# Kernel optimization log

Measured on AMD Instinct MI355X. Metric: run time of the kernel, lower is better.

## Reference

```python
import jax, jax.numpy as jnp
import numpy as np

B, S, D, H = 2, 2048, 1024, 16
HD = D // H  # head_size = 64

def setup_inputs() -> dict:
    key = jax.random.key(0)
    ks = jax.random.split(key, 8)
    sc = 0.02
    return {
        "q": jax.random.normal(ks[0], (B, S, D), jnp.float32),
        "k": jax.random.normal(ks[1], (B, S, D), jnp.float32),
        "v": jax.random.normal(ks[2], (B, S, D), jnp.float32),
        "padding_mask": jnp.zeros((B, 1, 1, S), jnp.float32),
        "Wq": jax.random.normal(ks[3], (D, D), jnp.float32) * sc,
        "bq": jnp.zeros((D,), jnp.float32),
        "Wk": jax.random.normal(ks[4], (D, D), jnp.float32) * sc,
        "bk": jnp.zeros((D,), jnp.float32),
        "Wv": jax.random.normal(ks[5], (D, D), jnp.float32) * sc,
        "bv": jnp.zeros((D,), jnp.float32),
        "Wo": jax.random.normal(ks[6], (D, D), jnp.float32) * sc,
        "bo": jnp.zeros((D,), jnp.float32),
    }

def reference(q, k, v, padding_mask, Wq, bq, Wk, bk, Wv, bv, Wo, bo):
    b = q.shape[0]
    qh = (q @ Wq + bq).reshape(b, -1, H, HD)
    kh = (k @ Wk + bk).reshape(b, -1, H, HD)
    vh = (v @ Wv + bv).reshape(b, -1, H, HD)
    # [B, H, Sq, Sk] scores, materialized as in the original
    qk = jnp.einsum('bjhd,bkhd->bhjk', qh, kh) / jnp.sqrt(jnp.float32(HD))
    qk = qk + padding_mask * -1e12
    attn = jax.nn.softmax(qk, axis=-1)
    qkv = jnp.einsum('bhjk,bkhd->bjhd', attn, vh).reshape(b, -1, D)
    return qkv @ Wo + bo
```

## Files before the change

### kernel.cpp

```cpp
#include <hip/hip_runtime.h>
#include <math.h>

typedef __bf16 bf16_t;
typedef __bf16 bf16x8 __attribute__((ext_vector_type(8)));
typedef __bf16 bf16x4v __attribute__((ext_vector_type(4)));
typedef float f32x4 __attribute__((ext_vector_type(4)));
typedef float f32x16 __attribute__((ext_vector_type(16)));

#define LOG2E 1.4426950408889634f
#define MBIAS_C (-1e12f * LOG2E)

#if __has_builtin(__builtin_amdgcn_exp2f)
#define EXP2F(x) __builtin_amdgcn_exp2f(x)
#else
#define EXP2F(x) exp2f(x)
#endif

typedef __attribute__((address_space(1))) const unsigned int g_u32;
typedef __attribute__((address_space(3))) unsigned int l_u32;
__device__ __forceinline__ void load_lds_16B(const void* g, void* l){
  __builtin_amdgcn_global_load_lds((g_u32*)g, (l_u32*)l, 16, 0, 0);
}

__device__ __forceinline__ f32x16 zero16(){
  f32x16 z;
  #pragma unroll
  for (int i = 0; i < 16; i++) z[i] = 0.f;
  return z;
}

typedef union { bf16x4v b4; uint2 u2; } pk8;
typedef union { uint2 h[2]; bf16x8 b8; } pk16;
typedef union { float4 f4[4]; f32x16 v; } cinit_t;

__global__ __launch_bounds__(256) void cast3_kernel(const float* __restrict__ q,
                                                    const float* __restrict__ k,
                                                    const float* __restrict__ v,
                                                    bf16_t* __restrict__ out){
  int z = blockIdx.y;
  const float* x = (z == 0) ? q : (z == 1) ? k : v;
  int i = blockIdx.x * 256 + threadIdx.x;
  float4 f = reinterpret_cast<const float4*>(x)[i];
  bf16x4v w;
  w[0] = (bf16_t)f.x; w[1] = (bf16_t)f.y; w[2] = (bf16_t)f.z; w[3] = (bf16_t)f.w;
  reinterpret_cast<bf16x4v*>(out + (size_t)z * 4194304)[i] = w;
}

__global__ __launch_bounds__(256) void mask_scale_kernel(const float* __restrict__ mask,
                                                         float* __restrict__ ms){
  int i = blockIdx.x * 256 + threadIdx.x;
  ms[i] = mask[i] * MBIAS_C;
}

__global__ __launch_bounds__(256) void wtrans4_kernel(const float* __restrict__ Wq,
                                                      const float* __restrict__ Wk,
                                                      const float* __restrict__ Wv,
                                                      const float* __restrict__ Wo,
                                                      bf16_t* __restrict__ Wcat,
                                                      bf16_t* __restrict__ Wot){
  __shared__ float T[32][33];
  int z = blockIdx.z;
  const float* W = (z == 0) ? Wq : (z == 1) ? Wk : (z == 2) ? Wv : Wo;
  bf16_t* dst = (z < 3) ? (Wcat + (size_t)z * 1024 * 1024) : Wot;
  int x = threadIdx.x, y = threadIdx.y;
  int k0 = blockIdx.y * 32, n0 = blockIdx.x * 32;
  #pragma unroll
  for (int i = 0; i < 4; i++) T[y + 8*i][x] = W[(size_t)(k0 + y + 8*i) * 1024 + n0 + x];
  __syncthreads();
  #pragma unroll
  for (int i = 0; i < 4; i++) dst[(size_t)(n0 + y + 8*i) * 1024 + k0 + x] = (bf16_t)T[x][y + 8*i];
}

__device__ __forceinline__ void qkv_epilogue(f32x4 (&acc)[4][4], int seg, int n0g, int m0,
                                             int wm, int wn, int l16, int lq,
                                             const float* bias, bf16_t* qp, bf16_t* kp,
                                             bf16_t* vh){
  bf16_t* Cp = (seg == 0) ? qp : (seg == 1) ? kp : vh;
  float scale = (seg == 0) ? 0.125f * LOG2E : 1.0f;
  #pragma unroll
  for (int ti = 0; ti < 4; ti++){
    #pragma unroll
    for (int tj = 0; tj < 4; tj++){
      int col = (n0g + wn + tj*16 + l16) & 1023;
      float bvv = bias[col];
      #pragma unroll
      for (int r = 0; r < 4; r++){
        int row = m0 + wm + ti*16 + lq*4 + r;
        Cp[(size_t)row * 1024 + col] = (bf16_t)((acc[ti][tj][r] + bvv) * scale);
      }
    }
  }
}

__global__ __launch_bounds__(256) void gemm_qkv_bf(const bf16_t* __restrict__ qkvin,
                                                   const bf16_t* __restrict__ Wcat,
                                                   const float* __restrict__ bq,
                                                   const float* __restrict__ bk,
                                                   const float* __restrict__ bv,
                                                   bf16_t* __restrict__ qp,
                                                   bf16_t* __restrict__ kp,
                                                   bf16_t* __restrict__ vh){
  const int K = 1024;
  __shared__ __align__(16) bf16_t As[128*32];
  __shared__ __align__(16) bf16_t Bs[128*32];
  int tid = threadIdx.x, wave = tid >> 6, lane = tid & 63;
  int l16 = lane & 15, lq = lane >> 4;
  int n0g = blockIdx.x * 128;
  int seg = n0g >> 10;
  const bf16_t* A   = qkvin + (size_t)seg * 4194304;
  const float* bias = (seg == 0) ? bq : (seg == 1) ? bk : bv;
  int m0 = blockIdx.y * 128;
  int wm = (wave >> 1) * 64, wn = (wave & 1) * 64;
  int cposR = lq ^ ((l16 >> 2) & 3);
  f32x4 acc[4][4] = {};
  for (int kt = 0; kt < K; kt += 32){
    __syncthreads();
    #pragma unroll
    for (int i = 0; i < 2; i++){
      int u = tid + 256*i;
      int r = u >> 2, cpos = u & 3, cg = cpos ^ ((r >> 2) & 3);
      int ldsoff = (wave*64 + 256*i) * 16;
      load_lds_16B(&A[(size_t)(m0 + r) * K + kt + cg*8], (char*)As + ldsoff);
      load_lds_16B(&Wcat[(size_t)(n0g + r) * K + kt + cg*8], (char*)Bs + ldsoff);
    }
    __syncthreads();
    bf16x8 af[4], bfr[4];
    #pragma unroll
    for (int t = 0; t < 4; t++) af[t]  = *reinterpret_cast<bf16x8*>(&As[(wm + t*16 + l16)*32 + cposR*8]);
    #pragma unroll
    for (int t = 0; t < 4; t++) bfr[t] = *reinterpret_cast<bf16x8*>(&Bs[(wn + t*16 + l16)*32 + cposR*8]);
    #pragma unroll
    for (int ti = 0; ti < 4; ti++)
      #pragma unroll
      for (int tj = 0; tj < 4; tj++)
        acc[ti][tj] = __builtin_amdgcn_mfma_f32_16x16x32_bf16(af[ti], bfr[tj], acc[ti][tj], 0, 0, 0);
  }
  qkv_epilogue(acc, seg, n0g, m0, wm, wn, l16, lq, bias, qp, kp, vh);
}

__global__ __launch_bounds__(256) void gemm_qkv_f32(const float* __restrict__ qi,
                                                    const float* __restrict__ ki,
                                                    const float* __restrict__ vi,
                                                    const bf16_t* __restrict__ Wcat,
                                                    const float* __restrict__ bq,
                                                    const float* __restrict__ bk,
                                                    const float* __restrict__ bv,
                                                    bf16_t* __restrict__ qp,
                                                    bf16_t* __restrict__ kp,
                                                    bf16_t* __restrict__ vh){
  const int K = 1024;
  __shared__ __align__(16) float  Asf[128*32];
  __shared__ __align__(16) bf16_t Bs[128*32];
  int tid = threadIdx.x, wave = tid >> 6, lane = tid & 63;
  int l16 = lane & 15, lq = lane >> 4;
  int n0g = blockIdx.x * 128;
  int seg = n0g >> 10;
  const float* A    = (seg == 0) ? qi : (seg == 1) ? ki : vi;
  const float* bias = (seg == 0) ? bq : (seg == 1) ? bk : bv;
  int m0 = blockIdx.y * 128;
  int wm = (wave >> 1) * 64, wn = (wave & 1) * 64;
  int cposR = lq ^ ((l16 >> 2) & 3);
  int ca0 = (2*lq)     ^ (l16 & 7);
  int ca1 = (2*lq + 1) ^ (l16 & 7);
  f32x4 acc[4][4] = {};
  for (int kt = 0; kt < K; kt += 32){
    __syncthreads();
    #pragma unroll
    for (int i = 0; i < 4; i++){
      int u = tid + 256*i;
      int r = u >> 3, cpos = u & 7, cg = cpos ^ (r & 7);
      load_lds_16B(&A[(size_t)(m0 + r) * K + kt + cg*4], (char*)Asf + (wave*64 + 256*i)*16);
    }
    #pragma unroll
    for (int i = 0; i < 2; i++){
      int u = tid + 256*i;
      int r = u >> 2, cpos = u & 3, cg = cpos ^ ((r >> 2) & 3);
      load_lds_16B(&Wcat[(size_t)(n0g + r) * K + kt + cg*8], (char*)Bs + (wave*64 + 256*i)*16);
    }
    __syncthreads();
    bf16x8 af[4], bfr[4];
    #pragma unroll
    for (int t = 0; t < 4; t++){
      int row = wm + t*16 + l16;
      f32x4 x0 = *reinterpret_cast<f32x4*>(&Asf[row*32 + ca0*4]);
      f32x4 x1 = *reinterpret_cast<f32x4*>(&Asf[row*32 + ca1*4]);
      bf16x8 a;
      a[0] = (bf16_t)x0[0]; a[1] = (bf16_t)x0[1]; a[2] = (bf16_t)x0[2]; a[3] = (bf16_t)x0[3];
      a[4] = (bf16_t)x1[0]; a[5] = (bf16_t)x1[1]; a[6] = (bf16_t)x1[2]; a[7] = (bf16_t)x1[3];
      af[t] = a;
    }
    #pragma unroll
    for (int t = 0; t < 4; t++) bfr[t] = *reinterpret_cast<bf16x8*>(&Bs[(wn + t*16 + l16)*32 + cposR*8]);
    #pragma unroll
    for (int ti = 0; ti < 4; ti++)
      #pragma unroll
      for (int tj = 0; tj < 4; tj++)
        acc[ti][tj] = __builtin_amdgcn_mfma_f32_16x16x32_bf16(af[ti], bfr[tj], acc[ti][tj], 0, 0, 0);
  }
  qkv_epilogue(acc, seg, n0g, m0, wm, wn, l16, lq, bias, qp, kp, vh);
}

__global__ __launch_bounds__(256) void gemm_out(const bf16_t* __restrict__ A,
                                                const bf16_t* __restrict__ Bt,
                                                const float* __restrict__ bias,
                                                float* __restrict__ C){
  const int K = 1024, N = 1024;
  __shared__ __align__(16) bf16_t As[128*64];
  __shared__ __align__(16) bf16_t Bs[64*64];
  int tid = threadIdx.x, wave = tid >> 6, lane = tid & 63;
  int l16 = lane & 15, lq = lane >> 4;
  int m0 = blockIdx.y * 128, n0 = blockIdx.x * 64;
  int wm = wave * 32;
  f32x4 acc[2][4] = {};
  for (int kt = 0; kt < K; kt += 64){
    __syncthreads();
    #pragma unroll
    for (int i = 0; i < 4; i++){
      int u = tid + 256*i;
      int r = u >> 3, cpos = u & 7, cg = cpos ^ (r & 7);
      load_lds_16B(&A[(size_t)(m0 + r) * K + kt + cg*8], (char*)As + (wave*64 + 256*i)*16);
    }
    #pragma unroll
    for (int i = 0; i < 2; i++){
      int u = tid + 256*i;
      int r = u >> 3, cpos = u & 7, cg = cpos ^ (r & 7);
      load_lds_16B(&Bt[(size_t)(n0 + r) * K + kt + cg*8], (char*)Bs + (wave*64 + 256*i)*16);
    }
    __syncthreads();
    #pragma unroll
    for (int kk = 0; kk < 2; kk++){
      bf16x8 af[2], bfr[4];
      #pragma unroll
      for (int t = 0; t < 2; t++){
        int row = wm + t*16 + l16, cpos = (kk*4 + lq) ^ (l16 & 7);
        af[t] = *reinterpret_cast<bf16x8*>(&As[row*64 + cpos*8]);
      }
      #pragma unroll
      for (int t = 0; t < 4; t++){
        int row = t*16 + l16, cpos = (kk*4 + lq) ^ (l16 & 7);
        bfr[t] = *reinterpret_cast<bf16x8*>(&Bs[row*64 + cpos*8]);
      }
      #pragma unroll
      for (int ti = 0; ti < 2; ti++)
        #pragma unroll
        for (int tj = 0; tj < 4; tj++)
          acc[ti][tj] = __builtin_amdgcn_mfma_f32_16x16x32_bf16(af[ti], bfr[tj], acc[ti][tj], 0, 0, 0);
    }
  }
  #pragma unroll
  for (int ti = 0; ti < 2; ti++){
    #pragma unroll
    for (int tj = 0; tj < 4; tj++){
      int col = n0 + tj*16 + l16;
      float bvv = bias[col];
      #pragma unroll
      for (int r = 0; r < 4; r++){
        int row = m0 + wm + ti*16 + lq*4 + r;
        C[(size_t)row * N + col] = acc[ti][tj][r] + bvv;
      }
    }
  }
}

__global__ __launch_bounds__(256) void vtrans_kernel(const bf16_t* __restrict__ vh,
                                                     bf16_t* __restrict__ Vt){
  __shared__ bf16_t T[64][72];
  int tid = threadIdx.x;
  int s0 = blockIdx.x * 64, h = blockIdx.y, b = blockIdx.z;
  #pragma unroll
  for (int i = 0; i < 2; i++){
    int u = tid + 256*i;
    int r = u >> 3, c = (u & 7) * 8;
    *reinterpret_cast<uint4*>(&T[r][c]) =
      *reinterpret_cast<const uint4*>(&vh[(size_t)(b*2048 + s0 + r) * 1024 + h*64 + c]);
  }
  __syncthreads();
  #pragma unroll
  for (int i = 0; i < 2; i++){
    int u = tid + 256*i;
    int d = u >> 3, cs = (u & 7) * 8;
    bf16_t t8[8];
    #pragma unroll
    for (int j = 0; j < 8; j++) t8[j] = T[cs + j][d];
    *reinterpret_cast<uint4*>(&Vt[(size_t)((b*16 + h)*64 + d) * 2048 + s0 + cs]) =
      *reinterpret_cast<uint4*>(t8);
  }
}

__global__ __launch_bounds__(512, 4) void attn_kernel(const bf16_t* __restrict__ qp,
                                                      const bf16_t* __restrict__ kp,
                                                      const bf16_t* __restrict__ vt,
                                                      const float* __restrict__ ms,
                                                      bf16_t* __restrict__ ctx){
  const int S = 2048, D = 1024, HD = 64;
  __shared__ __align__(16) char smem[74240];
  float* Lsum  = (float*)(smem + 73728);
  float* Opart = (float*)smem;
  const float* Ml = (const float*)(smem + 65536);
  int tid = threadIdx.x, wave = tid >> 6, lane = tid & 63;
  int l32 = lane & 31, H = lane >> 5;
  int qo = wave >> 1, khalf = wave & 1;
  int qt = blockIdx.x, h = blockIdx.y, b = blockIdx.z;
  const bf16_t* Qg = qp + (size_t)b*S*D + h*HD;
  const bf16_t* Kg = kp + (size_t)b*S*D + h*HD;
  const bf16_t* Vg = vt + (size_t)(b*16 + h)*HD*S;
  const float*  Mg = ms + (size_t)b*S;

  auto stage = [&](int kt, int bsel){
    char* Kd = smem + bsel*8192;
    char* Vd = smem + 32768 + bsel*8192;
    int r = tid >> 3, c = tid & 7, cg = c ^ (r & 7);
    int ldsoff = wave * 1024;
    load_lds_16B(&Kg[(size_t)(kt + r) * D + cg*8], Kd + ldsoff);
    load_lds_16B(&Vg[(size_t)r * S + kt + cg*8], Vd + ldsoff);
  };

  int qrow = qt*128 + qo*32 + l32;
  bf16x8 qf[4];
  #pragma unroll
  for (int s = 0; s < 4; s++)
    qf[s] = *reinterpret_cast<const bf16x8*>(&Qg[(size_t)qrow * D + s*16 + 8*H]);

  f32x16 o0 = zero16(), o1 = zero16(), lmm = zero16();
  int krow = khalf*32 + l32;

  pk16 ones;
  ones.h[0].x = 0x3F803F80u; ones.h[0].y = 0x3F803F80u;
  ones.h[1].x = 0x3F803F80u; ones.h[1].y = 0x3F803F80u;

  load_lds_16B(&Mg[(size_t)tid*4], smem + 65536 + wave*1024);
  stage(0, 0);
  stage(64, 1);
  __syncthreads();

  auto tile_compute = [&](int kt, int cur){
    bf16_t* Ks  = (bf16_t*)(smem + cur*8192);
    bf16_t* Vts = (bf16_t*)(smem + 32768 + cur*8192);
    cinit_t ci;
    #pragma unroll
    for (int g = 0; g < 4; g++)
      ci.f4[g] = *reinterpret_cast<const float4*>(&Ml[kt + khalf*32 + 8*g + 4*H]);
    f32x16 sc;
    __builtin_amdgcn_s_setprio(1);
    #pragma unroll
    for (int s = 0; s < 4; s++){
      int cp = (2*s + H) ^ (l32 & 7);
      bf16x8 kf = *reinterpret_cast<bf16x8*>(&Ks[krow*64 + cp*8]);
      if (s == 0) sc = __builtin_amdgcn_mfma_f32_32x32x16_bf16(kf, qf[0], ci.v, 0, 0, 0);
      else        sc = __builtin_amdgcn_mfma_f32_32x32x16_bf16(kf, qf[s], sc, 0, 0, 0);
    }
    __builtin_amdgcn_s_setprio(0);
    pk8 grp[4];
    #pragma unroll
    for (int g = 0; g < 4; g++){
      float p0 = EXP2F(sc[4*g+0]);
      float p1 = EXP2F(sc[4*g+1]);
      float p2 = EXP2F(sc[4*g+2]);
      float p3 = EXP2F(sc[4*g+3]);
      pk8 w;
      w.b4[0] = (bf16_t)p0; w.b4[1] = (bf16_t)p1; w.b4[2] = (bf16_t)p2; w.b4[3] = (bf16_t)p3;
      grp[g] = w;
    }
    #pragma unroll
    for (int kk = 0; kk < 2; kk++){
      uint2 ga = grp[2*kk].u2;
      uint2 gb = grp[2*kk+1].u2;
      uint2 send = H ? ga : gb;
      uint2 recv;
      recv.x = (unsigned)__shfl_xor((int)send.x, 32);
      recv.y = (unsigned)__shfl_xor((int)send.y, 32);
      pk16 fr;
      fr.h[0] = H ? recv : ga;
      fr.h[1] = H ? gb : recv;
      int cp = (4*khalf + 2*kk + H) ^ (l32 & 7);
      bf16x8 vf0 = *reinterpret_cast<bf16x8*>(&Vts[l32*64 + cp*8]);
      bf16x8 vf1 = *reinterpret_cast<bf16x8*>(&Vts[(32 + l32)*64 + cp*8]);
      __builtin_amdgcn_s_setprio(1);
      o0  = __builtin_amdgcn_mfma_f32_32x32x16_bf16(fr.b8, vf0, o0, 0, 0, 0);
      o1  = __builtin_amdgcn_mfma_f32_32x32x16_bf16(fr.b8, vf1, o1, 0, 0, 0);
      lmm = __builtin_amdgcn_mfma_f32_32x32x16_bf16(fr.b8, ones.b8, lmm, 0, 0, 0);
      __builtin_amdgcn_s_setprio(0);
    }
  };

  #pragma unroll 2
  for (int it = 0; it < 16; ++it){
    int kt = it * 128;
    if (it < 15){
      stage(kt + 128, (2*it + 2) & 3);
      stage(kt + 192, (2*it + 3) & 3);
    }
    tile_compute(kt,      (2*it) & 3);
    tile_compute(kt + 64, (2*it + 1) & 3);
    __syncthreads();
  }

  if (khalf == 1){
    #pragma unroll
    for (int reg = 0; reg < 16; reg++){
      Opart[qo*2048 + reg*64 + lane]        = o0[reg];
      Opart[qo*2048 + 1024 + reg*64 + lane] = o1[reg];
    }
    if (l32 == 0){
      #pragma unroll
      for (int reg = 0; reg < 16; reg++)
        Lsum[qo*32 + (reg & 3) + 8*(reg >> 2) + 4*H] = lmm[reg];
    }
  }
  __syncthreads();
  if (khalf == 0){
    #pragma unroll
    for (int reg = 0; reg < 16; reg++){
      o0[reg] += Opart[qo*2048 + reg*64 + lane];
      o1[reg] += Opart[qo*2048 + 1024 + reg*64 + lane];
    }
    #pragma unroll
    for (int g = 0; g < 4; g++){
      #pragma unroll
      for (int r = 0; r < 4; r++){
        float lf = lmm[4*g + r] + Lsum[qo*32 + 8*g + 4*H + r];
        float inv = 1.f / lf;
        int grow = qt*128 + qo*32 + 8*g + 4*H + r;
        size_t base = (size_t)(b*S + grow) * D + h*HD;
        ctx[base + l32]      = (bf16_t)(o0[4*g + r] * inv);
        ctx[base + 32 + l32] = (bf16_t)(o1[4*g + r] * inv);
      }
    }
  }
}

extern "C" void kernel_launch(void* const* d_in, const int* in_sizes, int n_in,
                              void* d_out, int out_size, void* d_ws, size_t ws_size,
                              hipStream_t stream){
  const float* q    = (const float*)d_in[0];
  const float* k    = (const float*)d_in[1];
  const float* v    = (const float*)d_in[2];
  const float* mask = (const float*)d_in[3];
  const float* Wq   = (const float*)d_in[4];
  const float* bq   = (const float*)d_in[5];
  const float* Wk   = (const float*)d_in[6];
  const float* bk   = (const float*)d_in[7];
  const float* Wv   = (const float*)d_in[8];
  const float* bv   = (const float*)d_in[9];
  const float* Wo   = (const float*)d_in[10];
  const float* bo   = (const float*)d_in[11];

  char* ws = (char*)d_ws;
  bf16_t* qp    = (bf16_t*)(ws);
  bf16_t* kp    = (bf16_t*)(ws + 8388608);
  bf16_t* vh    = (bf16_t*)(ws + 16777216);
  bf16_t* Wcat  = (bf16_t*)(ws + 25165824);
  bf16_t* Wot   = (bf16_t*)(ws + 31457280);
  bf16_t* Vt    = (bf16_t*)(ws + 33554432);
  bf16_t* ctx   = (bf16_t*)(ws + 41943040);
  bf16_t* qkvin = (bf16_t*)(ws + 33554432);
  float*  msbuf = (float*)(ws + 16777216);

  wtrans4_kernel<<<dim3(32,32,4), dim3(32,8), 0, stream>>>(Wq, Wk, Wv, Wo, Wcat, Wot);
  if (ws_size >= 58720256){
    cast3_kernel<<<dim3(4096,3), 256, 0, stream>>>(q, k, v, qkvin);
    gemm_qkv_bf<<<dim3(24,32), 256, 0, stream>>>(qkvin, Wcat, bq, bk, bv, qp, kp, vh);
  } else {
    gemm_qkv_f32<<<dim3(24,32), 256, 0, stream>>>(q, k, v, Wcat, bq, bk, bv, qp, kp, vh);
  }
  vtrans_kernel<<<dim3(32,16,2), 256, 0, stream>>>(vh, Vt);
  mask_scale_kernel<<<dim3(16), 256, 0, stream>>>(mask, msbuf);
  attn_kernel<<<dim3(16,16,2), 512, 0, stream>>>(qp, kp, Vt, msbuf, ctx);
  gemm_out<<<dim3(16,32), 256, 0, stream>>>(ctx, Wot, bo, (float*)d_out);
}
```

Before: 232.0 us.

## Fuse mask scaling into attention, deepen QKV GEMM K-tile, reorder grid mappings

Removes the separate mask_scale kernel launch by scaling the mask in LDS inside the attention kernel, at the cost of one extra barrier. Doubles the QKV GEMM K-tile from 32 to 64 with a new 8-way XOR swizzle, halving the loop iterations and barriers per block. Also swaps grid dimensions in the QKV GEMM, output GEMM and attention kernels so that neighbouring blocks share weight or head data, aiming for better L2 reuse.

After: 231.8 us. No clear change (-0.1%).

```diff
diff --git a/kernel.cpp b/kernel.cpp
--- a/kernel.cpp
+++ b/kernel.cpp
@@ -44,12 +44,6 @@
   bf16x4v w;
   w[0] = (bf16_t)f.x; w[1] = (bf16_t)f.y; w[2] = (bf16_t)f.z; w[3] = (bf16_t)f.w;
   reinterpret_cast<bf16x4v*>(out + (size_t)z * 4194304)[i] = w;
-}
-
-__global__ __launch_bounds__(256) void mask_scale_kernel(const float* __restrict__ mask,
-                                                         float* __restrict__ ms){
-  int i = blockIdx.x * 256 + threadIdx.x;
-  ms[i] = mask[i] * MBIAS_C;
 }
 
 __global__ __launch_bounds__(256) void wtrans4_kernel(const float* __restrict__ Wq,
@@ -101,39 +95,47 @@
                                                    bf16_t* __restrict__ kp,
                                                    bf16_t* __restrict__ vh){
   const int K = 1024;
-  __shared__ __align__(16) bf16_t As[128*32];
-  __shared__ __align__(16) bf16_t Bs[128*32];
+  __shared__ __align__(16) bf16_t As[128*64];
+  __shared__ __align__(16) bf16_t Bs[128*64];
   int tid = threadIdx.x, wave = tid >> 6, lane = tid & 63;
   int l16 = lane & 15, lq = lane >> 4;
-  int n0g = blockIdx.x * 128;
+  int m0  = blockIdx.x * 128;
+  int n0g = blockIdx.y * 128;
   int seg = n0g >> 10;
   const bf16_t* A   = qkvin + (size_t)seg * 4194304;
   const float* bias = (seg == 0) ? bq : (seg == 1) ? bk : bv;
-  int m0 = blockIdx.y * 128;
   int wm = (wave >> 1) * 64, wn = (wave & 1) * 64;
-  int cposR = lq ^ ((l16 >> 2) & 3);
   f32x4 acc[4][4] = {};
-  for (int kt = 0; kt < K; kt += 32){
-    __syncthreads();
-    #pragma unroll
-    for (int i = 0; i < 2; i++){
+  for (int kt = 0; kt < K; kt += 64){
+    __syncthreads();
+    #pragma unroll
+    for (int i = 0; i < 4; i++){
       int u = tid + 256*i;
-      int r = u >> 2, cpos = u & 3, cg = cpos ^ ((r >> 2) & 3);
+      int r = u >> 3, cpos = u & 7, cg = cpos ^ (r & 7);
       int ldsoff = (wave*64 + 256*i) * 16;
       load_lds_16B(&A[(size_t)(m0 + r) * K + kt + cg*8], (char*)As + ldsoff);
       load_lds_16B(&Wcat[(size_t)(n0g + r) * K + kt + cg*8], (char*)Bs + ldsoff);
     }
     __syncthreads();
-    bf16x8 af[4], bfr[4];
-    #pragma unroll
-    for (int t = 0; t < 4; t++) af[t]  = *reinterpret_cast<bf16x8*>(&As[(wm + t*16 + l16)*32 + cposR*8]);
-    #pragma unroll
-    for (int t = 0; t < 4; t++) bfr[t] = *reinterpret_cast<bf16x8*>(&Bs[(wn + t*16 + l16)*32 + cposR*8]);
-    #pragma unroll
-    for (int ti = 0; ti < 4; ti++)
-      #pragma unroll
-      for (int tj = 0; tj < 4; tj++)
-        acc[ti][tj] = __builtin_amdgcn_mfma_f32_16x16x32_bf16(af[ti], bfr[tj], acc[ti][tj], 0, 0, 0);
+    #pragma unroll
+    for (int kk = 0; kk < 2; kk++){
+      bf16x8 af[4], bfr[4];
+      #pragma unroll
+      for (int t = 0; t < 4; t++){
+        int row = wm + t*16 + l16, cpos = (kk*4 + lq) ^ (l16 & 7);
+        af[t] = *reinterpret_cast<bf16x8*>(&As[row*64 + cpos*8]);
+      }
+      #pragma unroll
+      for (int t = 0; t < 4; t++){
+        int row = wn + t*16 + l16, cpos = (kk*4 + lq) ^ (l16 & 7);
+        bfr[t] = *reinterpret_cast<bf16x8*>(&Bs[row*64 + cpos*8]);
+      }
+      #pragma unroll
+      for (int ti = 0; ti < 4; ti++)
+        #pragma unroll
+        for (int tj = 0; tj < 4; tj++)
+          acc[ti][tj] = __builtin_amdgcn_mfma_f32_16x16x32_bf16(af[ti], bfr[tj], acc[ti][tj], 0, 0, 0);
+    }
   }
   qkv_epilogue(acc, seg, n0g, m0, wm, wn, l16, lq, bias, qp, kp, vh);
 }
@@ -209,7 +211,7 @@
   __shared__ __align__(16) bf16_t Bs[64*64];
   int tid = threadIdx.x, wave = tid >> 6, lane = tid & 63;
   int l16 = lane & 15, lq = lane >> 4;
-  int m0 = blockIdx.y * 128, n0 = blockIdx.x * 64;
+  int m0 = blockIdx.x * 128, n0 = blockIdx.y * 64;
   int wm = wave * 32;
   f32x4 acc[2][4] = {};
   for (int kt = 0; kt < K; kt += 64){
@@ -290,21 +292,22 @@
 __global__ __launch_bounds__(512, 4) void attn_kernel(const bf16_t* __restrict__ qp,
                                                       const bf16_t* __restrict__ kp,
                                                       const bf16_t* __restrict__ vt,
-                                                      const float* __restrict__ ms,
+                                                      const float* __restrict__ mask,
                                                       bf16_t* __restrict__ ctx){
   const int S = 2048, D = 1024, HD = 64;
   __shared__ __align__(16) char smem[74240];
   float* Lsum  = (float*)(smem + 73728);
   float* Opart = (float*)smem;
-  const float* Ml = (const float*)(smem + 65536);
+  float* Mlw   = (float*)(smem + 65536);
+  const float* Ml = Mlw;
   int tid = threadIdx.x, wave = tid >> 6, lane = tid & 63;
   int l32 = lane & 31, H = lane >> 5;
   int qo = wave >> 1, khalf = wave & 1;
-  int qt = blockIdx.x, h = blockIdx.y, b = blockIdx.z;
+  int h = blockIdx.x, b = blockIdx.y, qt = blockIdx.z;
   const bf16_t* Qg = qp + (size_t)b*S*D + h*HD;
   const bf16_t* Kg = kp + (size_t)b*S*D + h*HD;
   const bf16_t* Vg = vt + (size_t)(b*16 + h)*HD*S;
-  const float*  Mg = ms + (size_t)b*S;
+  const float*  Mg = mask + (size_t)b*S;
 
   auto stage = [&](int kt, int bsel){
     char* Kd = smem + bsel*8192;
@@ -331,6 +334,12 @@
   load_lds_16B(&Mg[(size_t)tid*4], smem + 65536 + wave*1024);
   stage(0, 0);
   stage(64, 1);
+  __syncthreads();
+  {
+    f32x4 mv = *reinterpret_cast<f32x4*>(&Mlw[tid*4]);
+    mv *= MBIAS_C;
+    *reinterpret_cast<f32x4*>(&Mlw[tid*4]) = mv;
+  }
   __syncthreads();
 
   auto tile_compute = [&](int kt, int cur){
@@ -454,17 +463,15 @@
   bf16_t* Vt    = (bf16_t*)(ws + 33554432);
   bf16_t* ctx   = (bf16_t*)(ws + 41943040);
   bf16_t* qkvin = (bf16_t*)(ws + 33554432);
-  float*  msbuf = (float*)(ws + 16777216);
 
   wtrans4_kernel<<<dim3(32,32,4), dim3(32,8), 0, stream>>>(Wq, Wk, Wv, Wo, Wcat, Wot);
   if (ws_size >= 58720256){
     cast3_kernel<<<dim3(4096,3), 256, 0, stream>>>(q, k, v, qkvin);
-    gemm_qkv_bf<<<dim3(24,32), 256, 0, stream>>>(qkvin, Wcat, bq, bk, bv, qp, kp, vh);
+    gemm_qkv_bf<<<dim3(32,24), 256, 0, stream>>>(qkvin, Wcat, bq, bk, bv, qp, kp, vh);
   } else {
     gemm_qkv_f32<<<dim3(24,32), 256, 0, stream>>>(q, k, v, Wcat, bq, bk, bv, qp, kp, vh);
   }
   vtrans_kernel<<<dim3(32,16,2), 256, 0, stream>>>(vh, Vt);
-  mask_scale_kernel<<<dim3(16), 256, 0, stream>>>(mask, msbuf);
-  attn_kernel<<<dim3(16,16,2), 512, 0, stream>>>(qp, kp, Vt, msbuf, ctx);
-  gemm_out<<<dim3(16,32), 256, 0, stream>>>(ctx, Wot, bo, (float*)d_out);
-}
+  attn_kernel<<<dim3(16,2,16), 512, 0, stream>>>(qp, kp, Vt, mask, ctx);
+  gemm_out<<<dim3(32,16), 256, 0, stream>>>(ctx, Wot, bo, (float*)d_out);
+}
```
